# Kernel optimization log

Measured on AMD Instinct MI355X. Metric: run time of the kernel, lower is better.

The kernel has to match this reference:

```python
import jax, jax.numpy as jnp
import numpy as np

B, C_IN, T, N = 16, 64, 12, 1024
KS, C_OUT = 3, 64


def setup_inputs() -> dict:
    key = jax.random.key(0)
    k1, k2, k3 = jax.random.split(key, 3)
    x = jax.random.normal(k1, (B, C_IN, T, N), dtype=jnp.float32)
    # graph Chebyshev kernel [N, Ks*N]; scale down so matmuls stay well-conditioned
    kernel = jax.random.normal(k2, (N, KS * N), dtype=jnp.float32) / np.sqrt(N)
    # xavier-uniform theta [Ks*c_in, c_out]
    limit = np.sqrt(6.0 / (KS * C_IN + C_OUT))
    theta = jax.random.uniform(k3, (KS * C_IN, C_OUT), dtype=jnp.float32,
                               minval=-limit, maxval=limit)
    bias = jnp.zeros((C_OUT,), dtype=jnp.float32)
    return {"x": x, "kernel": kernel, "theta": theta, "bias": bias}


def reference(x, kernel, theta, bias):
    # x: [B, C, T, N]; kernel: [N, Ks*N] viewed as [N, Ks, N]; theta: [C*Ks, c_out]
    Bb, C, Tt, Nn = x.shape
    Ks = kernel.shape[1] // Nn
    Kr = kernel.reshape(Nn, Ks, Nn)            # [n, k, m]
    th = theta.reshape(C, Ks, -1)              # [c, k, o] (row index = c*Ks + k)
    # batched spectral conv over all timesteps at once (fuses the per-t loop)
    x_mul = jnp.einsum('bctn,nkm->bctkm', x, Kr)       # [B,C,T,Ks,N]
    gc = jnp.einsum('bctkm,cko->botm', x_mul, th)      # [B,c_out,T,N]
    gc = gc + bias[None, :, None, None]
    # c_in == c_out -> residual is identity
    return jax.nn.relu(gc + x)
```

## Files before the change

### kernel.cpp

```cpp
#include <hip/hip_runtime.h>

#define NB   16
#define NC   64
#define NT   12
#define NN   1024
#define NKS  3

typedef float  f32x4  __attribute__((ext_vector_type(4)));
typedef short  s16x8  __attribute__((ext_vector_type(8)));
typedef unsigned short u16x4 __attribute__((ext_vector_type(4)));
typedef unsigned short u16x8 __attribute__((ext_vector_type(8)));
typedef unsigned short ush;

__device__ __forceinline__ ush f2bf(float f) {
    union { float f; unsigned u; } v; v.f = f;
    unsigned r = v.u + 0x7FFFu + ((v.u >> 16) & 1u);
    return (ush)(r >> 16);
}
__device__ __forceinline__ float bf2f(ush h) {
    union { unsigned u; float f; } v; v.u = ((unsigned)h) << 16;
    return v.f;
}

__device__ __forceinline__ void cp16(const void* g, void* l) {
    __builtin_amdgcn_global_load_lds(
        (const __attribute__((address_space(1))) unsigned int*)g,
        (__attribute__((address_space(3))) unsigned int*)l, 16, 0, 0);
}

#define APAN_OFF 0
#define KB_OFF   25165824
#define TH_OFF   31457280

__global__ __launch_bounds__(256)
void spatio_prep(const float* __restrict__ x, const float* __restrict__ kern,
                 const float* __restrict__ theta,
                 ush* __restrict__ apan, ush* __restrict__ kb, ush* __restrict__ thbf)
{
    const int blk = blockIdx.x;
    const int tid = threadIdx.x;

    if (blk < 6144) {
        int id   = blk * 256 + tid;
        int slot = id & 511;
        int g2nb = id >> 9;
        int nb   = g2nb & 31, g2 = g2nb >> 5;
        int row  = slot >> 2, p = slot & 3;
        int d    = p ^ (row & 3);
        int bl   = row >> 6, c = row & 63;
        int bt   = 2 * g2 + bl;
        int b    = bt / NT, t = bt - NT * b;
        const float* src = x + ((size_t)((b * NC + c) * NT + t)) * NN + nb * 32 + d * 8;
        float4 a0 = ((const float4*)src)[0];
        float4 a1 = ((const float4*)src)[1];
        u16x8 w;
        w[0] = f2bf(a0.x); w[1] = f2bf(a0.y); w[2] = f2bf(a0.z); w[3] = f2bf(a0.w);
        w[4] = f2bf(a1.x); w[5] = f2bf(a1.y); w[6] = f2bf(a1.z); w[7] = f2bf(a1.w);
        ((u16x8*)apan)[id] = w;
    } else if (blk < 6528) {
        unsigned id2 = (unsigned)(blk - 6144) * 256u + (unsigned)tid;
        unsigned unit = id2 / 192u;
        int t    = (int)(id2 - unit * 192u);
        int mt   = (int)(unit >> 5), nb = (int)(unit & 31u);
        int k    = t >> 6, r = t & 63;
        int jqm  = r >> 2, d = r & 3;
        int colbase = (k << 10) + (mt << 6) + (jqm << 2);
        float4 v[8];
#pragma unroll
        for (int i = 0; i < 8; ++i)
            v[i] = *(const float4*)&kern[(size_t)(nb * 32 + d * 8 + i) * (NKS * NN) + colbase];
        int cbase = (mt * 32 + nb) * 768 + (k * 64 + jqm * 4) * 4;
#pragma unroll
        for (int jj = 0; jj < 4; ++jj) {
            u16x8 w;
            w[0] = f2bf(v[0][jj]); w[1] = f2bf(v[1][jj]);
            w[2] = f2bf(v[2][jj]); w[3] = f2bf(v[3][jj]);
            w[4] = f2bf(v[4][jj]); w[5] = f2bf(v[5][jj]);
            w[6] = f2bf(v[6][jj]); w[7] = f2bf(v[7][jj]);
            ((u16x8*)kb)[cbase + jj * 4 + (d ^ jj)] = w;
        }
    } else {
        int id = (blk - 6528) * 256 + tid;
        if (id < 12288) {
            int row = id >> 6, o = id & 63;
            int c = row / 3, k = row - 3 * c;
            thbf[o * 192 + k * 64 + c] = f2bf(theta[id]);
        }
    }
}

__global__ __launch_bounds__(256, 2)
void spatio_main(const ush* __restrict__ apan, const ush* __restrict__ kb,
                 const ush* __restrict__ thbf, const float* __restrict__ bias,
                 float* __restrict__ out)
{
    __shared__ __attribute__((aligned(128))) char smem[57344];
    ush (*xm)[200] = (ush (*)[200])smem;
    ush (*stL)[32] = (ush (*)[32])(smem + 40960);
    ush (*stH)[32] = (ush (*)[32])(smem + 49152);

    const int tid  = threadIdx.x;
    const int g2   = blockIdx.x;
    const int mt   = blockIdx.y;
    const int m_base = mt * 64;
    const int lane = tid & 63;
    const int wid  = tid >> 6;
    const int wr   = wid & 1;
    const int wn   = wid >> 1;
    const int quad = lane >> 4;
    const int l16  = lane & 15;
    const int pofs = (quad ^ (l16 & 3)) * 8;

    const char* apan_c = (const char*)apan + ((size_t)g2 << 18);
    const char* kb_c   = (const char*)kb + ((size_t)mt * 32 * 768 * 16);

    f32x4 acc[4][6];
#pragma unroll
    for (int i = 0; i < 4; ++i)
#pragma unroll
        for (int j = 0; j < 6; ++j) acc[i][j] = (f32x4){0.f, 0.f, 0.f, 0.f};

#pragma unroll
    for (int i = 0; i < 2; ++i)
        cp16(apan_c + (i * 256 + tid) * 16, smem + (i * 256 + tid) * 16);
#pragma unroll
    for (int i = 0; i < 3; ++i)
        cp16(kb_c + (i * 256 + tid) * 16, smem + 8192 + (i * 256 + tid) * 16);

    for (int it = 0; it < 32; ++it) {
        const int p = it & 1;
        char* buf = smem + p * 20480;
        __syncthreads();
        if (it < 31) {
            const char* asrc = apan_c + ((size_t)(it + 1) << 13);
            const char* bsrc = kb_c + (size_t)(it + 1) * 12288;
            char* nbuf = smem + (p ^ 1) * 20480;
#pragma unroll
            for (int i = 0; i < 2; ++i)
                cp16(asrc + (i * 256 + tid) * 16, nbuf + (i * 256 + tid) * 16);
#pragma unroll
            for (int i = 0; i < 3; ++i)
                cp16(bsrc + (i * 256 + tid) * 16, nbuf + 8192 + (i * 256 + tid) * 16);
        }
        if ((it >> 1) == mt) {
            const char* asrc = apan_c + ((size_t)it << 13);
            char* sb = smem + 40960 + (it & 1) * 8192;
#pragma unroll
            for (int i = 0; i < 2; ++i) {
                int m = i * 256 + tid;
                int slot = (m & ~3) + ((m & 3) ^ ((m >> 2) & 3));
                cp16(asrc + slot * 16, sb + m * 16);
            }
        }

        ush (*As)[32] = (ush (*)[32])buf;
        ush (*Bs)[32] = (ush (*)[32])(buf + 8192);
        s16x8 af[4], bf[6];
#pragma unroll
        for (int rb = 0; rb < 4; ++rb)
            af[rb] = *(const s16x8*)&As[64 * wr + 16 * rb + l16][pofs];
#pragma unroll
        for (int jb = 0; jb < 6; ++jb)
            bf[jb] = *(const s16x8*)&Bs[96 * wn + 16 * jb + l16][pofs];
#pragma unroll
        for (int rb = 0; rb < 4; ++rb)
#pragma unroll
            for (int jb = 0; jb < 6; ++jb)
                acc[rb][jb] = __builtin_amdgcn_mfma_f32_16x16x32_bf16(af[rb], bf[jb], acc[rb][jb], 0, 0, 0);
    }

    float bo[4];
#pragma unroll
    for (int r = 0; r < 4; ++r) bo[r] = bias[16 * wid + 4 * quad + r];

    for (int pass = 0; pass < 2; ++pass) {
        __syncthreads();
        if (wr == pass) {
#pragma unroll
            for (int rb = 0; rb < 4; ++rb)
#pragma unroll
                for (int jb = 0; jb < 6; ++jb) {
                    int J  = 96 * wn + 16 * jb + l16;
                    int kk = J >> 6, mm = J & 63;
                    int ck0 = kk * 64 + 16 * rb + 4 * quad;
                    u16x4 w;
                    w.x = f2bf(acc[rb][jb].x); w.y = f2bf(acc[rb][jb].y);
                    w.z = f2bf(acc[rb][jb].z); w.w = f2bf(acc[rb][jb].w);
                    *(u16x4*)&xm[mm][ck0] = w;
                }
        }
        __syncthreads();

        f32x4 acc2[4];
#pragma unroll
        for (int jb = 0; jb < 4; ++jb) acc2[jb] = (f32x4){0.f, 0.f, 0.f, 0.f};
#pragma unroll
        for (int ks = 0; ks < 6; ++ks) {
            s16x8 a2 = *(const s16x8*)(thbf + (size_t)(16 * wid + l16) * 192 + ks * 32 + quad * 8);
#pragma unroll
            for (int jb = 0; jb < 4; ++jb) {
                s16x8 b2 = *(const s16x8*)&xm[16 * jb + l16][ks * 32 + quad * 8];
                acc2[jb] = __builtin_amdgcn_mfma_f32_16x16x32_bf16(a2, b2, acc2[jb], 0, 0, 0);
            }
        }

        const int bt = 2 * g2 + pass;
        const int b2i = bt / NT, t2 = bt - NT * b2i;
#pragma unroll
        for (int jb = 0; jb < 4; ++jb) {
            int mm = 16 * jb + l16;
#pragma unroll
            for (int r = 0; r < 4; ++r) {
                int o = 16 * wid + 4 * quad + r;
                int row = pass * 64 + o;
                ush rv = (jb < 2) ? stL[row][mm] : stH[row][mm - 32];
                size_t idx = (((size_t)(b2i * NC + o) * NT + t2) * NN) + m_base + mm;
                float v = acc2[jb][r] + bo[r] + bf2f(rv);
                out[idx] = fmaxf(v, 0.f);
            }
        }
    }
}

extern "C" void kernel_launch(void* const* d_in, const int* in_sizes, int n_in,
                              void* d_out, int out_size, void* d_ws, size_t ws_size,
                              hipStream_t stream) {
    const float* x     = (const float*)d_in[0];
    const float* kern  = (const float*)d_in[1];
    const float* theta = (const float*)d_in[2];
    const float* bias  = (const float*)d_in[3];
    float* out = (float*)d_out;
    (void)in_sizes; (void)n_in; (void)out_size; (void)ws_size;

    ush* apan = (ush*)((char*)d_ws + APAN_OFF);
    ush* kbp  = (ush*)((char*)d_ws + KB_OFF);
    ush* thbf = (ush*)((char*)d_ws + TH_OFF);

    hipLaunchKernelGGL(spatio_prep, dim3(6576), dim3(256), 0, stream,
                       x, kern, theta, apan, kbp, thbf);
    hipLaunchKernelGGL(spatio_main, dim3(96, 16), dim3(256), 0, stream,
                       apan, kbp, thbf, bias, out);
}
```

Before: 189.5 us.

## Pre-pack operands in MFMA fragment order and load directly to registers

The prep kernel now writes the bf16 x panels and graph kernel in per-lane MFMA fragment order. This lets the main kernel load A and B fragments straight from global memory into registers with software double-buffering, and drops the LDS staging, double-buffer syncs and most of the shared memory. The residual is now read from fp32 x in global memory instead of from bf16 copies staged in LDS, which also makes it more exact. The intended gains are less LDS traffic, fewer barriers and higher occupancy. The cost is per-wave global loads with no reuse across waves, which leans on the L2 cache.

```diff
diff --git a/kernel.cpp b/kernel.cpp
--- a/kernel.cpp
+++ b/kernel.cpp
@@ -16,16 +16,6 @@
     union { float f; unsigned u; } v; v.f = f;
     unsigned r = v.u + 0x7FFFu + ((v.u >> 16) & 1u);
     return (ush)(r >> 16);
-}
-__device__ __forceinline__ float bf2f(ush h) {
-    union { unsigned u; float f; } v; v.u = ((unsigned)h) << 16;
-    return v.f;
-}
-
-__device__ __forceinline__ void cp16(const void* g, void* l) {
-    __builtin_amdgcn_global_load_lds(
-        (const __attribute__((address_space(1))) unsigned int*)g,
-        (__attribute__((address_space(3))) unsigned int*)l, 16, 0, 0);
 }
 
 #define APAN_OFF 0
@@ -42,15 +32,18 @@
 
     if (blk < 6144) {
         int id   = blk * 256 + tid;
-        int slot = id & 511;
-        int g2nb = id >> 9;
-        int nb   = g2nb & 31, g2 = g2nb >> 5;
-        int row  = slot >> 2, p = slot & 3;
-        int d    = p ^ (row & 3);
-        int bl   = row >> 6, c = row & 63;
-        int bt   = 2 * g2 + bl;
-        int b    = bt / NT, t = bt - NT * b;
-        const float* src = x + ((size_t)((b * NC + c) * NT + t)) * NN + nb * 32 + d * 8;
+        int lane = id & 63;
+        int fid  = (id >> 6) & 15;
+        int kt   = (id >> 10) & 15;
+        int g2   = id >> 14;
+        int quad = lane >> 4, l16 = lane & 15;
+        int wr = fid >> 3, rb = (fid >> 1) & 3, kk = fid & 1;
+        int row = 64 * wr + 16 * rb + l16;
+        int c = row & 63, bl = row >> 6;
+        int bt = 2 * g2 + bl;
+        int b = bt / NT, t = bt - NT * b;
+        int koff = kt * 64 + (kk * 4 + quad) * 8;
+        const float* src = x + ((size_t)((b * NC + c) * NT + t)) * NN + koff;
         float4 a0 = ((const float4*)src)[0];
         float4 a1 = ((const float4*)src)[1];
         u16x8 w;
@@ -58,18 +51,26 @@
         w[4] = f2bf(a1.x); w[5] = f2bf(a1.y); w[6] = f2bf(a1.z); w[7] = f2bf(a1.w);
         ((u16x8*)apan)[id] = w;
     } else if (blk < 6528) {
-        unsigned id2 = (unsigned)(blk - 6144) * 256u + (unsigned)tid;
-        unsigned unit = id2 / 192u;
-        int t    = (int)(id2 - unit * 192u);
-        int mt   = (int)(unit >> 5), nb = (int)(unit & 31u);
-        int k    = t >> 6, r = t & 63;
-        int jqm  = r >> 2, d = r & 3;
-        int colbase = (k << 10) + (mt << 6) + (jqm << 2);
+        int id   = (blk - 6144) * 256 + tid;
+        int quad = id & 3;
+        int l16g = (id >> 2) & 3;
+        int rest = id >> 4;
+        int jb   = rest % 6;
+        int r2   = rest / 6;
+        int kk   = r2 & 1;
+        int wn   = (r2 >> 1) & 1;
+        int kt   = (r2 >> 2) & 15;
+        int mt   = r2 >> 6;
+        int j0   = 96 * wn + 16 * jb + 4 * l16g;
+        int k    = j0 >> 6, mm0 = j0 & 63;
+        int col0 = (k << 10) + (mt << 6) + mm0;
+        int nbase = kt * 64 + (kk * 4 + quad) * 8;
         float4 v[8];
 #pragma unroll
         for (int i = 0; i < 8; ++i)
-            v[i] = *(const float4*)&kern[(size_t)(nb * 32 + d * 8 + i) * (NKS * NN) + colbase];
-        int cbase = (mt * 32 + nb) * 768 + (k * 64 + jqm * 4) * 4;
+            v[i] = *(const float4*)&kern[(size_t)(nbase + i) * (NKS * NN) + col0];
+        int fid = wn * 12 + kk * 6 + jb;
+        int cb  = ((mt * 16 + kt) * 24 + fid) * 64 + quad * 16 + 4 * l16g;
 #pragma unroll
         for (int jj = 0; jj < 4; ++jj) {
             u16x8 w;
@@ -77,7 +78,7 @@
             w[2] = f2bf(v[2][jj]); w[3] = f2bf(v[3][jj]);
             w[4] = f2bf(v[4][jj]); w[5] = f2bf(v[5][jj]);
             w[6] = f2bf(v[6][jj]); w[7] = f2bf(v[7][jj]);
-            ((u16x8*)kb)[cbase + jj * 4 + (d ^ jj)] = w;
+            ((u16x8*)kb)[cb + jj] = w;
         }
     } else {
         int id = (blk - 6528) * 256 + tid;
@@ -92,12 +93,10 @@
 __global__ __launch_bounds__(256, 2)
 void spatio_main(const ush* __restrict__ apan, const ush* __restrict__ kb,
                  const ush* __restrict__ thbf, const float* __restrict__ bias,
-                 float* __restrict__ out)
+                 const float* __restrict__ x, float* __restrict__ out)
 {
-    __shared__ __attribute__((aligned(128))) char smem[57344];
+    __shared__ __attribute__((aligned(128))) char smem[25600];
     ush (*xm)[200] = (ush (*)[200])smem;
-    ush (*stL)[32] = (ush (*)[32])(smem + 40960);
-    ush (*stH)[32] = (ush (*)[32])(smem + 49152);
 
     const int tid  = threadIdx.x;
     const int g2   = blockIdx.x;
@@ -109,10 +108,9 @@
     const int wn   = wid >> 1;
     const int quad = lane >> 4;
     const int l16  = lane & 15;
-    const int pofs = (quad ^ (l16 & 3)) * 8;
-
-    const char* apan_c = (const char*)apan + ((size_t)g2 << 18);
-    const char* kb_c   = (const char*)kb + ((size_t)mt * 32 * 768 * 16);
+
+    const ush* Abp = apan + (size_t)g2 * 131072 + wr * 4096 + lane * 8;
+    const ush* Bbp = kb   + (size_t)mt * 196608 + wn * 6144 + lane * 8;
 
     f32x4 acc[4][6];
 #pragma unroll
@@ -120,53 +118,38 @@
 #pragma unroll
         for (int j = 0; j < 6; ++j) acc[i][j] = (f32x4){0.f, 0.f, 0.f, 0.f};
 
-#pragma unroll
-    for (int i = 0; i < 2; ++i)
-        cp16(apan_c + (i * 256 + tid) * 16, smem + (i * 256 + tid) * 16);
-#pragma unroll
-    for (int i = 0; i < 3; ++i)
-        cp16(kb_c + (i * 256 + tid) * 16, smem + 8192 + (i * 256 + tid) * 16);
-
-    for (int it = 0; it < 32; ++it) {
-        const int p = it & 1;
-        char* buf = smem + p * 20480;
-        __syncthreads();
-        if (it < 31) {
-            const char* asrc = apan_c + ((size_t)(it + 1) << 13);
-            const char* bsrc = kb_c + (size_t)(it + 1) * 12288;
-            char* nbuf = smem + (p ^ 1) * 20480;
-#pragma unroll
-            for (int i = 0; i < 2; ++i)
-                cp16(asrc + (i * 256 + tid) * 16, nbuf + (i * 256 + tid) * 16);
-#pragma unroll
-            for (int i = 0; i < 3; ++i)
-                cp16(bsrc + (i * 256 + tid) * 16, nbuf + 8192 + (i * 256 + tid) * 16);
-        }
-        if ((it >> 1) == mt) {
-            const char* asrc = apan_c + ((size_t)it << 13);
-            char* sb = smem + 40960 + (it & 1) * 8192;
-#pragma unroll
-            for (int i = 0; i < 2; ++i) {
-                int m = i * 256 + tid;
-                int slot = (m & ~3) + ((m & 3) ^ ((m >> 2) & 3));
-                cp16(asrc + slot * 16, sb + m * 16);
-            }
-        }
-
-        ush (*As)[32] = (ush (*)[32])buf;
-        ush (*Bs)[32] = (ush (*)[32])(buf + 8192);
-        s16x8 af[4], bf[6];
+    s16x8 Pa[4], Pb[6], Qa[4], Qb[6];
+#pragma unroll
+    for (int rb = 0; rb < 4; ++rb) Pa[rb] = *(const s16x8*)(Abp + (rb * 2 + 0) * 512);
+#pragma unroll
+    for (int jb = 0; jb < 6; ++jb) Pb[jb] = *(const s16x8*)(Bbp + (0 * 6 + jb) * 512);
+
+    for (int h = 0; h < 32; h += 2) {
+        const int kt = h >> 1;
 #pragma unroll
         for (int rb = 0; rb < 4; ++rb)
-            af[rb] = *(const s16x8*)&As[64 * wr + 16 * rb + l16][pofs];
+            Qa[rb] = *(const s16x8*)(Abp + kt * 8192 + (rb * 2 + 1) * 512);
 #pragma unroll
         for (int jb = 0; jb < 6; ++jb)
-            bf[jb] = *(const s16x8*)&Bs[96 * wn + 16 * jb + l16][pofs];
+            Qb[jb] = *(const s16x8*)(Bbp + kt * 12288 + (6 + jb) * 512);
 #pragma unroll
         for (int rb = 0; rb < 4; ++rb)
 #pragma unroll
             for (int jb = 0; jb < 6; ++jb)
-                acc[rb][jb] = __builtin_amdgcn_mfma_f32_16x16x32_bf16(af[rb], bf[jb], acc[rb][jb], 0, 0, 0);
+                acc[rb][jb] = __builtin_amdgcn_mfma_f32_16x16x32_bf16(Pa[rb], Pb[jb], acc[rb][jb], 0, 0, 0);
+        if (h + 2 < 32) {
+#pragma unroll
+            for (int rb = 0; rb < 4; ++rb)
+                Pa[rb] = *(const s16x8*)(Abp + (kt + 1) * 8192 + (rb * 2) * 512);
+#pragma unroll
+            for (int jb = 0; jb < 6; ++jb)
+                Pb[jb] = *(const s16x8*)(Bbp + (kt + 1) * 12288 + jb * 512);
+        }
+#pragma unroll
+        for (int rb = 0; rb < 4; ++rb)
+#pragma unroll
+            for (int jb = 0; jb < 6; ++jb)
+                acc[rb][jb] = __builtin_amdgcn_mfma_f32_16x16x32_bf16(Qa[rb], Qb[jb], acc[rb][jb], 0, 0, 0);
     }
 
     float bo[4];
@@ -212,10 +195,8 @@
 #pragma unroll
             for (int r = 0; r < 4; ++r) {
                 int o = 16 * wid + 4 * quad + r;
-                int row = pass * 64 + o;
-                ush rv = (jb < 2) ? stL[row][mm] : stH[row][mm - 32];
                 size_t idx = (((size_t)(b2i * NC + o) * NT + t2) * NN) + m_base + mm;
-                float v = acc2[jb][r] + bo[r] + bf2f(rv);
+                float v = acc2[jb][r] + bo[r] + x[idx];
                 out[idx] = fmaxf(v, 0.f);
             }
         }
@@ -239,5 +220,5 @@
     hipLaunchKernelGGL(spatio_prep, dim3(6576), dim3(256), 0, stream,
                        x, kern, theta, apan, kbp, thbf);
     hipLaunchKernelGGL(spatio_main, dim3(96, 16), dim3(256), 0, stream,
-                       apan, kbp, thbf, bias, out);
-}
+                       apan, kbp, thbf, bias, x, out);
+}
```

Result: no change. 192.5 us (+1.6%).
